# Performance work log

Measured on AMD Instinct MI355X. Metric: run time of the kernel, lower is better.

Reference implementation:

```python
import jax, jax.numpy as jnp
import numpy as np

EMBED_DIM = 1024
NUM_HEADS = 16
KEY_SIZE = 1024
VALUE_SIZE = 1024
N, L = 4, 2048


def setup_inputs() -> dict:
    key = jax.random.key(0)
    ks = jax.random.split(key, 8)
    s = lambda fan_in: 1.0 / np.sqrt(fan_in)
    return {
        "x": jax.random.normal(ks[0], (N, L, EMBED_DIM), dtype=jnp.float32),
        # nn.Linear weights stored as (out, in); we apply x @ W.T
        "W_q": jax.random.uniform(ks[1], (KEY_SIZE, EMBED_DIM), jnp.float32, -s(EMBED_DIM), s(EMBED_DIM)),
        "W_k": jax.random.uniform(ks[2], (KEY_SIZE, EMBED_DIM), jnp.float32, -s(EMBED_DIM), s(EMBED_DIM)),
        "W_v": jax.random.uniform(ks[3], (VALUE_SIZE, EMBED_DIM), jnp.float32, -s(EMBED_DIM), s(EMBED_DIM)),
        "W_qp": jax.random.uniform(ks[4], (KEY_SIZE, KEY_SIZE), jnp.float32, -s(KEY_SIZE), s(KEY_SIZE)),
        "W_kp": jax.random.uniform(ks[5], (KEY_SIZE, KEY_SIZE), jnp.float32, -s(KEY_SIZE), s(KEY_SIZE)),
        "W_vp": jax.random.uniform(ks[6], (VALUE_SIZE, VALUE_SIZE), jnp.float32, -s(VALUE_SIZE), s(VALUE_SIZE)),
        "W_out": jax.random.uniform(ks[7], (EMBED_DIM, VALUE_SIZE), jnp.float32, -s(VALUE_SIZE), s(VALUE_SIZE)),
    }


def reference(x, W_q, W_k, W_v, W_qp, W_kp, W_vp, W_out):
    H = NUM_HEADS
    q = (x @ W_q.T) @ W_qp.T   # (N, L, key_size)
    k = (x @ W_k.T) @ W_kp.T   # (N, L, key_size)
    v = (x @ W_v.T) @ W_vp.T   # (N, L, value_size)
    n, l, vs = v.shape
    dq = q.shape[-1] // H
    dv = vs // H
    q = q.reshape(n, l, H, dq).transpose(0, 2, 1, 3)  # (N, H, L, dq)
    k = k.reshape(n, l, H, dq).transpose(0, 2, 1, 3)
    v = v.reshape(n, l, H, dv).transpose(0, 2, 1, 3)
    att = jnp.einsum("nhid,nhjd->nhij", q, k) / jnp.sqrt(jnp.float32(dq))
    att = jax.nn.softmax(att, axis=-1)
    out = jnp.einsum("nhij,nhjd->nhid", att, v)       # (N, H, L, dv)
    out = out.transpose(0, 2, 1, 3).reshape(n, l, vs)
    return out @ W_out.T
```

## Files before the change

kernel.cpp:

```cpp
#include <hip/hip_runtime.h>
#include <cstddef>
#include <cstdint>

#define EMBED 1024
#define NH    16
#define DQ    64
#define NB    4
#define LSEQ  2048
#define MROWS (NB * LSEQ)

typedef __bf16 bf16x8 __attribute__((ext_vector_type(8)));
typedef float  f32x4  __attribute__((ext_vector_type(4)));

__device__ __forceinline__ unsigned short f2bf(float f) {
    return (unsigned short)((__float_as_uint(f) + 0x8000u) >> 16);
}

__device__ __forceinline__ unsigned pack2(float a, float b) {
    unsigned ua = __float_as_uint(a) + 0x8000u;
    unsigned ub = __float_as_uint(b) + 0x8000u;
    return __builtin_amdgcn_perm(ub, ua, 0x07060302u);
}

__device__ __forceinline__ uint2 pack4(float a, float b, float c, float d) {
    return make_uint2(pack2(a, b), pack2(c, d));
}

__device__ __forceinline__ unsigned pack2t(float a, float b) {
    return __builtin_amdgcn_perm(__float_as_uint(b), __float_as_uint(a), 0x07060302u);
}

__device__ __forceinline__ void async_cp16(const void* g, void* l) {
    __builtin_amdgcn_global_load_lds((const __attribute__((address_space(1))) unsigned int*)g,
                                     (__attribute__((address_space(3))) unsigned int*)l,
                                     16, 0, 0);
}

struct CvtJobs {
    const float* src[8];
    unsigned short* dst[8];
    int n[8];
};

__global__ __launch_bounds__(256) void cvt_bf16(CvtJobs j) {
    int job = blockIdx.y;
    const float* s = j.src[job];
    unsigned short* d = j.dst[job];
    int n4 = j.n[job] >> 2;
    int stride = gridDim.x * blockDim.x;
    for (int i = blockIdx.x * blockDim.x + threadIdx.x; i < n4; i += stride) {
        float4 f = ((const float4*)s)[i];
        ((uint2*)d)[i] = pack4(f.x, f.y, f.z, f.w);
    }
}

struct TransJobs {
    const float* src[3];
    unsigned short* dst[3];
};

__global__ __launch_bounds__(256) void transpose_cvt(TransJobs tj) {
    __shared__ unsigned short Ts[64][68];
    const float* src = tj.src[blockIdx.z];
    unsigned short* dst = tj.dst[blockIdx.z];
    const int tid = threadIdx.x;
    const int r0 = blockIdx.y * 64;
    const int c0 = blockIdx.x * 64;

    {
        int col4 = tid & 15;
        int rb   = tid >> 4;
#pragma unroll
        for (int it = 0; it < 4; it++) {
            int r = rb + it * 16;
            float4 f = *(const float4*)(src + (size_t)(r0 + r) * 1024 + c0 + col4 * 4);
            *(uint2*)&Ts[r][col4 * 4] = pack4(f.x, f.y, f.z, f.w);
        }
    }
    __syncthreads();

    {
        int oc = tid >> 2;
        int seg = tid & 3;
        __attribute__((aligned(16))) unsigned short tmp[16];
#pragma unroll
        for (int e = 0; e < 16; e++) tmp[e] = Ts[seg * 16 + e][oc];
        unsigned short* out = dst + (size_t)(c0 + oc) * 1024 + r0 + seg * 16;
        *(uint4*)(out)     = *(const uint4*)&tmp[0];
        *(uint4*)(out + 8) = *(const uint4*)&tmp[8];
    }
}

struct BGemmArgs {
    const unsigned short* A[3];
    const unsigned short* B[3];
    void* C[3];
    int mode[3];
    float scl[3];
};

__global__ __launch_bounds__(256, 4) void gemm_bf16nt(BGemmArgs p, int M, int N, int K) {
    __shared__ __align__(16) unsigned short SMEM[2 * 128 * 64];
    unsigned short* As = SMEM;
    unsigned short* Bs = SMEM + 128 * 64;

    const int tid  = threadIdx.x;
    const int wave = tid >> 6;
    const int lane = tid & 63;
    const int m16  = lane & 15;
    const int kq   = lane >> 4;

    const int nwg  = gridDim.x * gridDim.y;
    const int flat = blockIdx.y * gridDim.x + blockIdx.x;
    const int swz  = (flat & 7) * (nwg >> 3) + (flat >> 3);
    const int bm = (swz / gridDim.x) * 128;
    const int bn = (swz % gridDim.x) * 128;
    const int z  = blockIdx.z;
    const unsigned short* A = p.A[z];
    const unsigned short* B = p.B[z];

    f32x4 acc[4][4];
#pragma unroll
    for (int i = 0; i < 4; i++)
#pragma unroll
        for (int j = 0; j < 4; j++) acc[i][j] = f32x4{0.f, 0.f, 0.f, 0.f};

    const int wr = (wave >> 1) * 64;
    const int wc = (wave & 1) * 64;

    for (int k0 = 0; k0 < K; k0 += 64) {
#pragma unroll
        for (int it = 0; it < 4; it++) {
            int c = tid + it * 256;
            int r = c >> 3;
            int kc = (c & 7) ^ (r & 7);
            async_cp16(A + (size_t)(bm + r) * K + k0 + kc * 8,
                       &As[(it * 256 + wave * 64) * 8]);
            async_cp16(B + (size_t)(bn + r) * K + k0 + kc * 8,
                       &Bs[(it * 256 + wave * 64) * 8]);
        }
        __syncthreads();

#pragma unroll
        for (int s = 0; s < 2; s++) {
            bf16x8 af[4], bfr[4];
#pragma unroll
            for (int i = 0; i < 4; i++) {
                int ra = wr + i * 16 + m16;
                af[i] = *reinterpret_cast<const bf16x8*>(
                    &As[ra * 64 + (((s * 4 + kq) ^ (ra & 7)) * 8)]);
                int rb = wc + i * 16 + m16;
                bfr[i] = *reinterpret_cast<const bf16x8*>(
                    &Bs[rb * 64 + (((s * 4 + kq) ^ (rb & 7)) * 8)]);
            }
#pragma unroll
            for (int i = 0; i < 4; i++)
#pragma unroll
                for (int j = 0; j < 4; j++)
                    acc[i][j] = __builtin_amdgcn_mfma_f32_16x16x32_bf16(af[i], bfr[j], acc[i][j], 0, 0, 0);
        }
        __syncthreads();
    }

    const int mode = p.mode[z];
    const float scl = p.scl[z];
    if (mode == 0) {
        unsigned short* Cb = (unsigned short*)p.C[z];
#pragma unroll
        for (int i = 0; i < 4; i++)
#pragma unroll
            for (int j = 0; j < 4; j++) {
                int row = bm + wr + i * 16 + kq * 4;
                int col = bn + wc + j * 16 + m16;
#pragma unroll
                for (int q = 0; q < 4; q++)
                    Cb[(size_t)(row + q) * N + col] = f2bf(acc[i][j][q] * scl);
            }
    } else if (mode == 1) {
        float* Cf = (float*)p.C[z];
#pragma unroll
        for (int i = 0; i < 4; i++)
#pragma unroll
            for (int j = 0; j < 4; j++) {
                int row = bm + wr + i * 16 + kq * 4;
                int col = bn + wc + j * 16 + m16;
#pragma unroll
                for (int q = 0; q < 4; q++)
                    Cf[(size_t)(row + q) * N + col] = acc[i][j][q];
            }
    } else {
        unsigned short* Tt = SMEM;
#pragma unroll
        for (int i = 0; i < 4; i++)
#pragma unroll
            for (int j = 0; j < 4; j++) {
                int c = wc + j * 16 + m16;
                int u = (wr >> 2) + i * 4 + kq;
                int us = (u + 2 * c) & 31;
                *reinterpret_cast<uint2*>(&Tt[c * 128 + us * 4]) =
                    pack4(acc[i][j][0], acc[i][j][1], acc[i][j][2], acc[i][j][3]);
            }
        __syncthreads();
        unsigned short* Ct = (unsigned short*)p.C[z];
        int r8 = tid & 15;
        int cb = tid >> 4;
#pragma unroll
        for (int pass = 0; pass < 8; pass++) {
            int c  = pass * 16 + cb;
            int u0 = r8 * 2;
            int us = (u0 + 2 * c) & 31;
            uint4 val = *reinterpret_cast<const uint4*>(&Tt[c * 128 + us * 4]);
            int key0 = r8 * 8;
            int loc  = key0 & 31;
            int dst0 = (key0 & 96) + (((loc & 15) >> 2) * 8) + ((loc >> 4) * 4);
            unsigned short* out = &Ct[(size_t)(bn + c) * M + bm + dst0];
            *reinterpret_cast<uint2*>(out)     = make_uint2(val.x, val.y);
            *reinterpret_cast<uint2*>(out + 8) = make_uint2(val.z, val.w);
        }
    }
}

__global__ __launch_bounds__(256, 4)
void flash_bf16(const unsigned short* __restrict__ qb,
                const unsigned short* __restrict__ kb,
                const unsigned short* __restrict__ vtb,
                unsigned short* __restrict__ ao) {
    __shared__ __align__(16) unsigned short Ks[2][64 * 64];
    __shared__ __align__(16) unsigned short Vt[2][64 * 64];

    const int tid  = threadIdx.x;
    const int wave = tid >> 6;
    const int lane = tid & 63;
    const int m16  = lane & 15;
    const int kq   = lane >> 4;

    const int flat = blockIdx.y * (LSEQ / 128) + blockIdx.x;
    const int swz  = (flat & 7) * 128 + (flat >> 3);
    const int bh   = swz >> 4;
    const int nn   = bh >> 4;
    const int h    = bh & 15;
    const int q0   = (swz & 15) * 128;

    const uint4 ones_u = make_uint4(0x3F803F80u, 0x3F803F80u, 0x3F803F80u, 0x3F803F80u);
    const bf16x8 ones8 = __builtin_bit_cast(bf16x8, ones_u);

    const unsigned short* kptr  = kb + (size_t)(nn * LSEQ) * EMBED + h * DQ;
    const unsigned short* vtptr = vtb + (size_t)(h * DQ) * MROWS + nn * LSEQ;

    auto stage = [&](int buf) {
#pragma unroll
        for (int it = 0; it < 2; it++) {
            int c = tid + it * 256;
            int r = c >> 3;
            int kc = (c & 7) ^ (r & 7);
            async_cp16(kptr + (size_t)r * EMBED + kc * 8,
                       &Ks[buf][(it * 256 + wave * 64) * 8]);
            async_cp16(vtptr + (size_t)r * MROWS + kc * 8,
                       &Vt[buf][(it * 256 + wave * 64) * 8]);
        }
        kptr  += 64 * EMBED;
        vtptr += 64;
    };

    stage(0);

    bf16x8 qf[2][2];
#pragma unroll
    for (int j = 0; j < 2; j++) {
        size_t tok = (size_t)(nn * LSEQ + q0 + wave * 32 + j * 16 + m16);
#pragma unroll
        for (int s = 0; s < 2; s++)
            qf[j][s] = *reinterpret_cast<const bf16x8*>(
                &qb[tok * EMBED + h * DQ + s * 32 + kq * 8]);
    }

    f32x4 o[4][2];
    f32x4 o4[2];
#pragma unroll
    for (int j = 0; j < 2; j++) {
        o4[j] = f32x4{0.f, 0.f, 0.f, 0.f};
#pragma unroll
        for (int mt = 0; mt < 4; mt++) o[mt][j] = f32x4{0.f, 0.f, 0.f, 0.f};
    }

    asm volatile("s_waitcnt vmcnt(0)" ::: "memory");
    __builtin_amdgcn_s_barrier();
    asm volatile("" ::: "memory");

    const int NT = LSEQ / 64;
    for (int kt = 0; kt < NT; kt++) {
        const int cur = kt & 1;
        if (kt + 1 < NT) stage(cur ^ 1);

        f32x4 st[4][2];
#pragma unroll
        for (int i = 0; i < 4; i++)
#pragma unroll
            for (int j = 0; j < 2; j++) st[i][j] = f32x4{0.f, 0.f, 0.f, 0.f};

#pragma unroll
        for (int s = 0; s < 2; s++) {
            bf16x8 ak[4];
#pragma unroll
            for (int i = 0; i < 4; i++) {
                int key = i * 16 + m16;
                ak[i] = *reinterpret_cast<const bf16x8*>(
                    &Ks[cur][key * 64 + (((s * 4 + kq) ^ (m16 & 7)) * 8)]);
            }
            __builtin_amdgcn_s_setprio(1);
#pragma unroll
            for (int i = 0; i < 4; i++)
#pragma unroll
                for (int j = 0; j < 2; j++)
                    st[i][j] = __builtin_amdgcn_mfma_f32_16x16x32_bf16(ak[i], qf[j][s], st[i][j], 0, 0, 0);
            __builtin_amdgcn_s_setprio(0);
        }

#pragma unroll
        for (int t = 0; t < 2; t++) {
            bf16x8 av8[4];
#pragma unroll
            for (int mt = 0; mt < 4; mt++) {
                int d = mt * 16 + m16;
                av8[mt] = *reinterpret_cast<const bf16x8*>(
                    &Vt[cur][d * 64 + (((t * 4 + kq) ^ (m16 & 7)) * 8)]);
            }
#pragma unroll
            for (int ii = 0; ii < 2; ii++)
#pragma unroll
                for (int j = 0; j < 2; j++)
#pragma unroll
                    for (int q = 0; q < 4; q++)
                        st[2 * t + ii][j][q] = __builtin_amdgcn_exp2f(st[2 * t + ii][j][q]);
            bf16x8 pb[2];
#pragma unroll
            for (int j = 0; j < 2; j++) {
                uint4 pu;
                pu.x = pack2t(st[2 * t][j][0],     st[2 * t][j][1]);
                pu.y = pack2t(st[2 * t][j][2],     st[2 * t][j][3]);
                pu.z = pack2t(st[2 * t + 1][j][0], st[2 * t + 1][j][1]);
                pu.w = pack2t(st[2 * t + 1][j][2], st[2 * t + 1][j][3]);
                pb[j] = __builtin_bit_cast(bf16x8, pu);
            }
            __builtin_amdgcn_s_setprio(1);
#pragma unroll
            for (int mt = 0; mt < 4; mt++)
#pragma unroll
                for (int j = 0; j < 2; j++)
                    o[mt][j] = __builtin_amdgcn_mfma_f32_16x16x32_bf16(av8[mt], pb[j], o[mt][j], 0, 0, 0);
#pragma unroll
            for (int j = 0; j < 2; j++)
                o4[j] = __builtin_amdgcn_mfma_f32_16x16x32_bf16(ones8, pb[j], o4[j], 0, 0, 0);
            __builtin_amdgcn_s_setprio(0);
        }

        if (kt + 1 < NT) {
            asm volatile("s_waitcnt vmcnt(0)" ::: "memory");
            __builtin_amdgcn_s_barrier();
            asm volatile("" ::: "memory");
        }
    }

#pragma unroll
    for (int j = 0; j < 2; j++) {
        float inv = 1.f / o4[j][0];
        size_t tok = (size_t)(nn * LSEQ + q0 + wave * 32 + j * 16 + m16);
#pragma unroll
        for (int mt = 0; mt < 4; mt++) {
            *reinterpret_cast<uint2*>(&ao[tok * EMBED + h * DQ + mt * 16 + kq * 4]) =
                pack4(o[mt][j][0] * inv, o[mt][j][1] * inv, o[mt][j][2] * inv, o[mt][j][3] * inv);
        }
    }
}

extern "C" void kernel_launch(void* const* d_in, const int* in_sizes, int n_in,
                              void* d_out, int out_size, void* d_ws, size_t ws_size,
                              hipStream_t stream) {
    (void)in_sizes; (void)n_in; (void)out_size; (void)ws_size;
    const float* x     = (const float*)d_in[0];
    const float* W_q   = (const float*)d_in[1];
    const float* W_k   = (const float*)d_in[2];
    const float* W_v   = (const float*)d_in[3];
    const float* W_qp  = (const float*)d_in[4];
    const float* W_kp  = (const float*)d_in[5];
    const float* W_vp  = (const float*)d_in[6];
    const float* W_out = (const float*)d_in[7];

    unsigned short* ws16 = (unsigned short*)d_ws;
    const size_t SZX = (size_t)MROWS * EMBED;
    const size_t SZW = (size_t)EMBED * EMBED;

    unsigned short* xb    = ws16;
    unsigned short* wqpb  = xb + SZX;
    unsigned short* wkpb  = wqpb + SZW;
    unsigned short* wvpb  = wkpb + SZW;
    unsigned short* woutb = wvpb + SZW;
    unsigned short* wqT   = woutb + SZW;
    unsigned short* wkT   = wqT + SZW;
    unsigned short* wvT   = wkT + SZW;
    unsigned short* weq   = wvT + SZW;
    unsigned short* wek   = weq + SZW;
    unsigned short* wev   = wek + SZW;
    unsigned short* qbuf  = wev + SZW;
    unsigned short* kbuf  = qbuf + SZX;
    unsigned short* vtbuf = kbuf + SZX;
    unsigned short* ao    = vtbuf + SZX;

    CvtJobs cj;
    cj.src[0] = x;     cj.dst[0] = xb;    cj.n[0] = (int)SZX;
    cj.src[1] = W_qp;  cj.dst[1] = wqpb;  cj.n[1] = (int)SZW;
    cj.src[2] = W_kp;  cj.dst[2] = wkpb;  cj.n[2] = (int)SZW;
    cj.src[3] = W_vp;  cj.dst[3] = wvpb;  cj.n[3] = (int)SZW;
    cj.src[4] = W_out; cj.dst[4] = woutb; cj.n[4] = (int)SZW;
    cvt_bf16<<<dim3(512, 5), 256, 0, stream>>>(cj);

    TransJobs tj;
    tj.src[0] = W_q; tj.src[1] = W_k; tj.src[2] = W_v;
    tj.dst[0] = wqT; tj.dst[1] = wkT; tj.dst[2] = wvT;
    transpose_cvt<<<dim3(16, 16, 3), 256, 0, stream>>>(tj);

    BGemmArgs fz;
    fz.A[0] = wqpb; fz.A[1] = wkpb; fz.A[2] = wvpb;
    fz.B[0] = wqT;  fz.B[1] = wkT;  fz.B[2] = wvT;
    fz.C[0] = weq;  fz.C[1] = wek;  fz.C[2] = wev;
    fz.mode[0] = 0; fz.mode[1] = 0; fz.mode[2] = 0;
    fz.scl[0] = 1.f; fz.scl[1] = 1.f; fz.scl[2] = 1.f;
    gemm_bf16nt<<<dim3(8, 8, 3), 256, 0, stream>>>(fz, EMBED, EMBED, EMBED);

    BGemmArgs pj;
    pj.A[0] = xb;   pj.A[1] = xb;   pj.A[2] = xb;
    pj.B[0] = weq;  pj.B[1] = wek;  pj.B[2] = wev;
    pj.C[0] = qbuf; pj.C[1] = kbuf; pj.C[2] = vtbuf;
    pj.mode[0] = 0; pj.mode[1] = 0; pj.mode[2] = 2;
    pj.scl[0] = 0.18033688f; pj.scl[1] = 1.f; pj.scl[2] = 1.f;
    gemm_bf16nt<<<dim3(8, 64, 3), 256, 0, stream>>>(pj, MROWS, EMBED, EMBED);

    flash_bf16<<<dim3(LSEQ / 128, NB * NH), 256, 0, stream>>>(qbuf, kbuf, vtbuf, ao);

    BGemmArgs og;
    og.A[0] = ao;    og.A[1] = ao;    og.A[2] = ao;
    og.B[0] = woutb; og.B[1] = woutb; og.B[2] = woutb;
    og.C[0] = d_out; og.C[1] = d_out; og.C[2] = d_out;
    og.mode[0] = 1; og.mode[1] = 1; og.mode[2] = 1;
    og.scl[0] = 1.f; og.scl[1] = 1.f; og.scl[2] = 1.f;
    gemm_bf16nt<<<dim3(8, 64, 1), 256, 0, stream>>>(og, MROWS, EMBED, EMBED);
}
```

Measured before the change: 273.5 us.

## Merge weight prep kernels and overlap x conversion with weight-fusion GEMM

Combines the weight bf16 conversion and the transpose-conversion into a single prep kernel. The large x conversion moves into extra blocks of the small weight-product GEMM launch, so it runs alongside a GEMM that only fills 192 blocks. In the flash kernel, the first QK MFMA now takes a zero accumulator directly instead of zero-initialising the score registers separately. This removes one launch and uses idle CUs, at the cost of the mixed-role launch being bound by the GEMM's launch bounds and shared-memory size.

Measured after the change: 273.5 us. No clear change (+0.0%).

```diff
diff --git a/kernel.cpp b/kernel.cpp
--- a/kernel.cpp
+++ b/kernel.cpp
@@ -36,58 +36,52 @@
                                      16, 0, 0);
 }
 
-struct CvtJobs {
-    const float* src[8];
-    unsigned short* dst[8];
-    int n[8];
+struct PrepArgs {
+    const float* tsrc[3];
+    unsigned short* tdst[3];
+    const float* csrc[4];
+    unsigned short* cdst[4];
 };
 
-__global__ __launch_bounds__(256) void cvt_bf16(CvtJobs j) {
-    int job = blockIdx.y;
-    const float* s = j.src[job];
-    unsigned short* d = j.dst[job];
-    int n4 = j.n[job] >> 2;
-    int stride = gridDim.x * blockDim.x;
-    for (int i = blockIdx.x * blockDim.x + threadIdx.x; i < n4; i += stride) {
-        float4 f = ((const float4*)s)[i];
-        ((uint2*)d)[i] = pack4(f.x, f.y, f.z, f.w);
-    }
-}
-
-struct TransJobs {
-    const float* src[3];
-    unsigned short* dst[3];
-};
-
-__global__ __launch_bounds__(256) void transpose_cvt(TransJobs tj) {
-    __shared__ unsigned short Ts[64][68];
-    const float* src = tj.src[blockIdx.z];
-    unsigned short* dst = tj.dst[blockIdx.z];
+__global__ __launch_bounds__(256) void prep_all(PrepArgs pa) {
     const int tid = threadIdx.x;
-    const int r0 = blockIdx.y * 64;
-    const int c0 = blockIdx.x * 64;
-
-    {
-        int col4 = tid & 15;
-        int rb   = tid >> 4;
-#pragma unroll
-        for (int it = 0; it < 4; it++) {
-            int r = rb + it * 16;
-            float4 f = *(const float4*)(src + (size_t)(r0 + r) * 1024 + c0 + col4 * 4);
-            *(uint2*)&Ts[r][col4 * 4] = pack4(f.x, f.y, f.z, f.w);
-        }
-    }
-    __syncthreads();
-
-    {
-        int oc = tid >> 2;
-        int seg = tid & 3;
-        __attribute__((aligned(16))) unsigned short tmp[16];
-#pragma unroll
-        for (int e = 0; e < 16; e++) tmp[e] = Ts[seg * 16 + e][oc];
-        unsigned short* out = dst + (size_t)(c0 + oc) * 1024 + r0 + seg * 16;
-        *(uint4*)(out)     = *(const uint4*)&tmp[0];
-        *(uint4*)(out + 8) = *(const uint4*)&tmp[8];
+    if (blockIdx.z < 3) {
+        __shared__ unsigned short Ts[64][68];
+        const float* src = pa.tsrc[blockIdx.z];
+        unsigned short* dst = pa.tdst[blockIdx.z];
+        const int r0 = blockIdx.y * 64;
+        const int c0 = blockIdx.x * 64;
+        {
+            int col4 = tid & 15;
+            int rb   = tid >> 4;
+#pragma unroll
+            for (int it = 0; it < 4; it++) {
+                int r = rb + it * 16;
+                float4 f = *(const float4*)(src + (size_t)(r0 + r) * 1024 + c0 + col4 * 4);
+                *(uint2*)&Ts[r][col4 * 4] = pack4(f.x, f.y, f.z, f.w);
+            }
+        }
+        __syncthreads();
+        {
+            int oc = tid >> 2;
+            int seg = tid & 3;
+            __attribute__((aligned(16))) unsigned short tmp[16];
+#pragma unroll
+            for (int e = 0; e < 16; e++) tmp[e] = Ts[seg * 16 + e][oc];
+            unsigned short* out = dst + (size_t)(c0 + oc) * 1024 + r0 + seg * 16;
+            *(uint4*)(out)     = *(const uint4*)&tmp[0];
+            *(uint4*)(out + 8) = *(const uint4*)&tmp[8];
+        }
+    } else {
+        int job = blockIdx.z - 3;
+        const float* s = pa.csrc[job];
+        unsigned short* d = pa.cdst[job];
+        const int n4 = (1024 * 1024) >> 2;
+        int flat = blockIdx.y * 16 + blockIdx.x;
+        for (int i = flat * 256 + tid; i < n4; i += 256 * 256) {
+            float4 f = ((const float4*)s)[i];
+            ((uint2*)d)[i] = pack4(f.x, f.y, f.z, f.w);
+        }
     }
 }
 
@@ -99,8 +93,8 @@
     float scl[3];
 };
 
-__global__ __launch_bounds__(256, 4) void gemm_bf16nt(BGemmArgs p, int M, int N, int K) {
-    __shared__ __align__(16) unsigned short SMEM[2 * 128 * 64];
+__device__ __forceinline__ void gemm_core(const BGemmArgs& p, int M, int N, int K,
+                                          unsigned short* SMEM) {
     unsigned short* As = SMEM;
     unsigned short* Bs = SMEM + 128 * 64;
 
@@ -220,6 +214,35 @@
     }
 }
 
+__global__ __launch_bounds__(256, 4) void gemm_bf16nt(BGemmArgs p, int M, int N, int K) {
+    __shared__ __align__(16) unsigned short SMEM[2 * 128 * 64];
+    gemm_core(p, M, N, K, SMEM);
+}
+
+struct FuseXArgs {
+    BGemmArgs g;
+    const float* xsrc;
+    unsigned short* xdst;
+};
+
+__global__ __launch_bounds__(256, 4) void gemm_fuse_xcvt(FuseXArgs fa) {
+    if (blockIdx.z < 3) {
+        __shared__ __align__(16) unsigned short SMEM[2 * 128 * 64];
+        gemm_core(fa.g, 1024, 1024, 1024, SMEM);
+    } else {
+        const int n4 = (MROWS * EMBED) >> 2;
+        int slice = blockIdx.z - 3;
+        int flat  = blockIdx.y * gridDim.x + blockIdx.x;
+        int start = (slice * 64 + flat) * 256 + threadIdx.x;
+        const float4* s = (const float4*)fa.xsrc;
+        uint2* d = (uint2*)fa.xdst;
+        for (int i = start; i < n4; i += 192 * 256) {
+            float4 f = s[i];
+            d[i] = pack4(f.x, f.y, f.z, f.w);
+        }
+    }
+}
+
 __global__ __launch_bounds__(256, 4)
 void flash_bf16(const unsigned short* __restrict__ qb,
                 const unsigned short* __restrict__ kb,
@@ -282,6 +305,7 @@
 #pragma unroll
         for (int mt = 0; mt < 4; mt++) o[mt][j] = f32x4{0.f, 0.f, 0.f, 0.f};
     }
+    const f32x4 zero4 = f32x4{0.f, 0.f, 0.f, 0.f};
 
     asm volatile("s_waitcnt vmcnt(0)" ::: "memory");
     __builtin_amdgcn_s_barrier();
@@ -294,11 +318,6 @@
 
         f32x4 st[4][2];
 #pragma unroll
-        for (int i = 0; i < 4; i++)
-#pragma unroll
-            for (int j = 0; j < 2; j++) st[i][j] = f32x4{0.f, 0.f, 0.f, 0.f};
-
-#pragma unroll
         for (int s = 0; s < 2; s++) {
             bf16x8 ak[4];
 #pragma unroll
@@ -308,11 +327,19 @@
                     &Ks[cur][key * 64 + (((s * 4 + kq) ^ (m16 & 7)) * 8)]);
             }
             __builtin_amdgcn_s_setprio(1);
-#pragma unroll
-            for (int i = 0; i < 4; i++)
-#pragma unroll
-                for (int j = 0; j < 2; j++)
-                    st[i][j] = __builtin_amdgcn_mfma_f32_16x16x32_bf16(ak[i], qf[j][s], st[i][j], 0, 0, 0);
+            if (s == 0) {
+#pragma unroll
+                for (int i = 0; i < 4; i++)
+#pragma unroll
+                    for (int j = 0; j < 2; j++)
+                        st[i][j] = __builtin_amdgcn_mfma_f32_16x16x32_bf16(ak[i], qf[j][0], zero4, 0, 0, 0);
+            } else {
+#pragma unroll
+                for (int i = 0; i < 4; i++)
+#pragma unroll
+                    for (int j = 0; j < 2; j++)
+                        st[i][j] = __builtin_amdgcn_mfma_f32_16x16x32_bf16(ak[i], qf[j][1], st[i][j], 0, 0, 0);
+            }
             __builtin_amdgcn_s_setprio(0);
         }
 
@@ -406,26 +433,24 @@
     unsigned short* vtbuf = kbuf + SZX;
     unsigned short* ao    = vtbuf + SZX;
 
-    CvtJobs cj;
-    cj.src[0] = x;     cj.dst[0] = xb;    cj.n[0] = (int)SZX;
-    cj.src[1] = W_qp;  cj.dst[1] = wqpb;  cj.n[1] = (int)SZW;
-    cj.src[2] = W_kp;  cj.dst[2] = wkpb;  cj.n[2] = (int)SZW;
-    cj.src[3] = W_vp;  cj.dst[3] = wvpb;  cj.n[3] = (int)SZW;
-    cj.src[4] = W_out; cj.dst[4] = woutb; cj.n[4] = (int)SZW;
-    cvt_bf16<<<dim3(512, 5), 256, 0, stream>>>(cj);
-
-    TransJobs tj;
-    tj.src[0] = W_q; tj.src[1] = W_k; tj.src[2] = W_v;
-    tj.dst[0] = wqT; tj.dst[1] = wkT; tj.dst[2] = wvT;
-    transpose_cvt<<<dim3(16, 16, 3), 256, 0, stream>>>(tj);
-
-    BGemmArgs fz;
-    fz.A[0] = wqpb; fz.A[1] = wkpb; fz.A[2] = wvpb;
-    fz.B[0] = wqT;  fz.B[1] = wkT;  fz.B[2] = wvT;
-    fz.C[0] = weq;  fz.C[1] = wek;  fz.C[2] = wev;
-    fz.mode[0] = 0; fz.mode[1] = 0; fz.mode[2] = 0;
-    fz.scl[0] = 1.f; fz.scl[1] = 1.f; fz.scl[2] = 1.f;
-    gemm_bf16nt<<<dim3(8, 8, 3), 256, 0, stream>>>(fz, EMBED, EMBED, EMBED);
+    PrepArgs pa;
+    pa.tsrc[0] = W_q;  pa.tsrc[1] = W_k;  pa.tsrc[2] = W_v;
+    pa.tdst[0] = wqT;  pa.tdst[1] = wkT;  pa.tdst[2] = wvT;
+    pa.csrc[0] = W_qp;  pa.cdst[0] = wqpb;
+    pa.csrc[1] = W_kp;  pa.cdst[1] = wkpb;
+    pa.csrc[2] = W_vp;  pa.cdst[2] = wvpb;
+    pa.csrc[3] = W_out; pa.cdst[3] = woutb;
+    prep_all<<<dim3(16, 16, 7), 256, 0, stream>>>(pa);
+
+    FuseXArgs fx;
+    fx.g.A[0] = wqpb; fx.g.A[1] = wkpb; fx.g.A[2] = wvpb;
+    fx.g.B[0] = wqT;  fx.g.B[1] = wkT;  fx.g.B[2] = wvT;
+    fx.g.C[0] = weq;  fx.g.C[1] = wek;  fx.g.C[2] = wev;
+    fx.g.mode[0] = 0; fx.g.mode[1] = 0; fx.g.mode[2] = 0;
+    fx.g.scl[0] = 1.f; fx.g.scl[1] = 1.f; fx.g.scl[2] = 1.f;
+    fx.xsrc = x;
+    fx.xdst = xb;
+    gemm_fuse_xcvt<<<dim3(8, 8, 6), 256, 0, stream>>>(fx);
 
     BGemmArgs pj;
     pj.A[0] = xb;   pj.A[1] = xb;   pj.A[2] = xb;
```
